# Optimization experiments

Measured on AMD Instinct MI355X. Metric: run time of the kernel, lower is better.

Reference implementation:

```python
import jax, jax.numpy as jnp
import numpy as np

B, C, D, Q = 256, 1000, 128, 262144
PROTO_M = 0.99   # args.proto_m
TEMP = 0.01      # hardcoded temperature in forward


def setup_inputs() -> dict:
    key = jax.random.key(0)
    ks = jax.random.split(key, 8)
    return {
        'q': jax.random.normal(ks[0], (B, D), jnp.float32),
        'k': jax.random.normal(ks[1], (B, D), jnp.float32),
        'output': jax.random.normal(ks[2], (B, C), jnp.float32),
        'output2': jax.random.normal(ks[3], (B, C), jnp.float32),
        'partial_Y': (jax.random.uniform(ks[4], (B, C)) < 0.1).astype(jnp.float32),
        'prototypes': jax.random.normal(ks[5], (C, D), jnp.float32),
        'queue': jax.random.normal(ks[6], (Q, D), jnp.float32),
        'queue_pseudo': jax.random.uniform(ks[7], (Q,), dtype=jnp.float32),
    }


def reference(q, k, output, output2, partial_Y, prototypes, queue, queue_pseudo):
    # pseudo-label selection: softmax over (detached logits * candidate mask) / T
    predicted_scores = jax.nn.softmax(jax.lax.stop_gradient(output) * partial_Y / TEMP, axis=1)
    pseudo_labels_b = jnp.argmax(predicted_scores, axis=1)  # [B] int

    # prototype scores use prototypes BEFORE the EMA update (mm snapshots values)
    logits_prot = jnp.matmul(jax.lax.stop_gradient(q), prototypes.T)  # [B, C]
    score_prot = jax.nn.softmax(logits_prot, axis=1)

    # sequential per-sample EMA scatter into prototypes (order-dependent on dup labels)
    q_detached = jax.lax.stop_gradient(q)

    def ema_step(protos, xs):
        feat, lab = xs
        new_row = protos[lab] * PROTO_M + (1.0 - PROTO_M) * feat
        return protos.at[lab].set(new_row), None

    protos, _ = jax.lax.scan(ema_step, prototypes, (q_detached, pseudo_labels_b))
    # F.normalize(p=2, dim=1) with eps=1e-12 clamp
    protos = protos / jnp.maximum(jnp.linalg.norm(protos, axis=1, keepdims=True), 1e-12)

    features = jnp.concatenate([q, k, queue], axis=0)  # [2B+Q, D]
    pseudo_labels = jnp.concatenate([
        pseudo_labels_b.astype(jnp.float32),
        pseudo_labels_b.astype(jnp.float32),
        queue_pseudo,
    ], axis=0)  # [2B+Q]

    return (output, output2, features, pseudo_labels, score_prot, protos)
```

## Files before the change

### kernel.cpp

```cpp
#include <hip/hip_runtime.h>
#include <math.h>

#define B 256
#define C 1000
#define D 128
#define QN 262144

#define OFF_FEAT   512000
#define OFF_LBL    34131968
#define OFF_SCORE  34394624
#define OFF_PROTO  34650624

#define N_Q4   (QN * D / 4)
#define N_O4   (B * C / 4)
#define N_F4   (B * D / 4)
#define N_P4   (QN / 4)

#define DST_Q4   ((OFF_FEAT + 2 * B * D) / 4)
#define DST_O24  (B * C / 4)
#define DST_QF4  (OFF_FEAT / 4)
#define DST_KF4  (OFF_FEAT / 4 + N_F4)
#define DST_P4   ((OFF_LBL + 2 * B) / 4)

#define SM_O2  (N_O4)
#define SM_Q   (2 * N_O4)
#define SM_K   (2 * N_O4 + N_F4)
#define SM_P   (2 * N_O4 + 2 * N_F4)
#define SM_TOT (2 * N_O4 + 2 * N_F4 + N_P4)

#define Q_TILES   (N_Q4 / 1024)
#define K1_TILES  640
#define POOL_BASE4 ((size_t)K1_TILES * 1024)
#define POOL_N4    ((size_t)(Q_TILES - K1_TILES) * 1024)

#define R_SP_END  256
#define R_EMA_END (R_SP_END + 250)
#define SM_BLKS   ((SM_TOT + 255) / 256)
#define R_SM_END  (R_EMA_END + SM_BLKS)
#define K2_GRID   2048
#define TOT_THR   ((size_t)K2_GRID * 256)

__global__ __launch_bounds__(256) void k1_kernel(
    const float* __restrict__ output,
    const float* __restrict__ partial_Y,
    const float4* __restrict__ queue,
    int* __restrict__ labels,
    float* __restrict__ out)
{
    const int tid = threadIdx.x;

    if (blockIdx.x >= B) {
        const size_t base = (size_t)(blockIdx.x - B) * 1024 + tid;
        float4* __restrict__ dst = (float4*)out + DST_Q4;
        float4 a = queue[base];
        float4 b = queue[base + 256];
        float4 c = queue[base + 512];
        float4 d = queue[base + 768];
        dst[base]       = a;
        dst[base + 256] = b;
        dst[base + 512] = c;
        dst[base + 768] = d;
        return;
    }

    const int b = blockIdx.x;
    const float* row = output + (size_t)b * C;
    const float* msk = partial_Y + (size_t)b * C;

    float best = -INFINITY;
    int bidx = C;
    for (int c = tid; c < C; c += 256) {
        float v = row[c] * msk[c];
        if (v > best) { best = v; bidx = c; }
    }

    __shared__ float sv[256];
    __shared__ int   si[256];
    sv[tid] = best; si[tid] = bidx;
    __syncthreads();
    for (int s = 128; s > 0; s >>= 1) {
        if (tid < s) {
            float v2 = sv[tid + s]; int i2 = si[tid + s];
            if (v2 > sv[tid] || (v2 == sv[tid] && i2 < si[tid])) {
                sv[tid] = v2; si[tid] = i2;
            }
        }
        __syncthreads();
    }
    if (tid == 0) {
        int lab = si[0];
        labels[b] = lab;
        float f = (float)lab;
        out[OFF_LBL + b]     = f;
        out[OFF_LBL + B + b] = f;
    }
}

__global__ __launch_bounds__(256) void k2_kernel(
    const float* __restrict__ q,
    const float* __restrict__ kk,
    const float* __restrict__ output,
    const float* __restrict__ output2,
    const float* __restrict__ prototypes,
    const float4* __restrict__ queue,
    const float* __restrict__ queue_pseudo,
    const int* __restrict__ labels,
    float* __restrict__ out)
{
    const int bid = blockIdx.x;
    const int tid = threadIdx.x;

    __shared__ float logits[C];
    __shared__ float red[256];
    __shared__ float qs[D];
    __shared__ int   lab[B];
    __shared__ float ss[256];

    if (bid < R_SP_END) {
        const int b = bid;
        if (tid < D) qs[tid] = q[(size_t)b * D + tid];
        __syncthreads();

        for (int c = tid; c < C; c += 256) {
            const float4* p4 = (const float4*)(prototypes + (size_t)c * D);
            const float4* q4 = (const float4*)qs;
            float acc = 0.f;
            #pragma unroll
            for (int d = 0; d < D / 4; ++d) {
                float4 pv = p4[d];
                float4 qv = q4[d];
                acc += pv.x * qv.x + pv.y * qv.y + pv.z * qv.z + pv.w * qv.w;
            }
            logits[c] = acc;
        }
        __syncthreads();

        float lm = -INFINITY;
        for (int c = tid; c < C; c += 256) lm = fmaxf(lm, logits[c]);
        red[tid] = lm;
        __syncthreads();
        for (int s = 128; s > 0; s >>= 1) {
            if (tid < s) red[tid] = fmaxf(red[tid], red[tid + s]);
            __syncthreads();
        }
        const float m = red[0];
        __syncthreads();

        float psum = 0.f;
        for (int c = tid; c < C; c += 256) {
            float e = expf(logits[c] - m);
            logits[c] = e;
            psum += e;
        }
        red[tid] = psum;
        __syncthreads();
        for (int s = 128; s > 0; s >>= 1) {
            if (tid < s) red[tid] += red[tid + s];
            __syncthreads();
        }
        const float denom = red[0];

        for (int c = tid; c < C; c += 256)
            out[OFF_SCORE + (size_t)b * C + c] = logits[c] / denom;
    }
    else if (bid < R_EMA_END) {
        const int ebid = bid - R_SP_END;
        const int half = tid >> 7;
        const int d    = tid & 127;
        for (int i = tid; i < B; i += 256) lab[i] = labels[i];
        __syncthreads();

        #pragma unroll
        for (int kcl = 0; kcl < 2; ++kcl) {
            const int c = 4 * ebid + 2 * kcl + half;
            float val = prototypes[(size_t)c * D + d];
            #pragma unroll 8
            for (int b = 0; b < B; ++b) {
                if (lab[b] == c) {
                    val = val * 0.99f + 0.01f * q[(size_t)b * D + d];
                }
            }
            ss[tid] = val * val;
            __syncthreads();
            for (int s = 64; s > 0; s >>= 1) {
                if (d < s) ss[tid] += ss[tid + s];
                __syncthreads();
            }
            float r = fmaxf(sqrtf(ss[half * 128]), 1e-12f);
            out[OFF_PROTO + (size_t)c * D + d] = val / r;
            __syncthreads();
        }
    }
    else if (bid < R_SM_END) {
        const size_t i = (size_t)(bid - R_EMA_END) * 256 + tid;
        float4* __restrict__ out4 = (float4*)out;
        if (i < SM_O2)       out4[i]                     = ((const float4*)output)[i];
        else if (i < SM_Q)   out4[DST_O24 + (i - SM_O2)] = ((const float4*)output2)[i - SM_O2];
        else if (i < SM_K)   out4[DST_QF4 + (i - SM_Q)]  = ((const float4*)q)[i - SM_Q];
        else if (i < SM_P)   out4[DST_KF4 + (i - SM_K)]  = ((const float4*)kk)[i - SM_K];
        else if (i < SM_TOT) out4[DST_P4 + (i - SM_P)]   = ((const float4*)queue_pseudo)[i - SM_P];
    }

    const float4* __restrict__ srcq = queue + POOL_BASE4;
    float4* __restrict__ dstq = (float4*)out + DST_Q4 + POOL_BASE4;
    const size_t gid = (size_t)bid * 256 + tid;
    size_t i = gid;
    for (; i + 3 * TOT_THR < POOL_N4; i += 4 * TOT_THR) {
        float4 a = srcq[i];
        float4 b = srcq[i +     TOT_THR];
        float4 c = srcq[i + 2 * TOT_THR];
        float4 d = srcq[i + 3 * TOT_THR];
        dstq[i]               = a;
        dstq[i +     TOT_THR] = b;
        dstq[i + 2 * TOT_THR] = c;
        dstq[i + 3 * TOT_THR] = d;
    }
    for (; i < POOL_N4; i += TOT_THR)
        dstq[i] = srcq[i];
}

extern "C" void kernel_launch(void* const* d_in, const int* in_sizes, int n_in,
                              void* d_out, int out_size, void* d_ws, size_t ws_size,
                              hipStream_t stream) {
    const float* q            = (const float*)d_in[0];
    const float* k            = (const float*)d_in[1];
    const float* output       = (const float*)d_in[2];
    const float* output2      = (const float*)d_in[3];
    const float* partial_Y    = (const float*)d_in[4];
    const float* prototypes   = (const float*)d_in[5];
    const float* queue        = (const float*)d_in[6];
    const float* queue_pseudo = (const float*)d_in[7];

    float* out  = (float*)d_out;
    int* labels = (int*)d_ws;

    k1_kernel<<<B + K1_TILES, 256, 0, stream>>>(
        output, partial_Y, (const float4*)queue, labels, out);

    k2_kernel<<<K2_GRID, 256, 0, stream>>>(
        q, k, output, output2, prototypes,
        (const float4*)queue, queue_pseudo, labels, out);
}
```

Before: 270.7 us.

## Split work into three kernels: independent work first, EMA, then queue copy

```diff
diff --git a/kernel.cpp b/kernel.cpp
--- a/kernel.cpp
+++ b/kernel.cpp
@@ -33,91 +33,68 @@
 #define POOL_BASE4 ((size_t)K1_TILES * 1024)
 #define POOL_N4    ((size_t)(Q_TILES - K1_TILES) * 1024)
 
-#define R_SP_END  256
-#define R_EMA_END (R_SP_END + 250)
+#define R1_SP     256
+#define R1_SM     512
 #define SM_BLKS   ((SM_TOT + 255) / 256)
-#define R_SM_END  (R_EMA_END + SM_BLKS)
-#define K2_GRID   2048
-#define TOT_THR   ((size_t)K2_GRID * 256)
+#define R1_CP     (R1_SM + SM_BLKS)
+#define K1_GRID   (R1_CP + K1_TILES)
+
+#define K3_GRID   4096
 
 __global__ __launch_bounds__(256) void k1_kernel(
-    const float* __restrict__ output,
-    const float* __restrict__ partial_Y,
-    const float4* __restrict__ queue,
-    int* __restrict__ labels,
-    float* __restrict__ out)
-{
-    const int tid = threadIdx.x;
-
-    if (blockIdx.x >= B) {
-        const size_t base = (size_t)(blockIdx.x - B) * 1024 + tid;
-        float4* __restrict__ dst = (float4*)out + DST_Q4;
-        float4 a = queue[base];
-        float4 b = queue[base + 256];
-        float4 c = queue[base + 512];
-        float4 d = queue[base + 768];
-        dst[base]       = a;
-        dst[base + 256] = b;
-        dst[base + 512] = c;
-        dst[base + 768] = d;
-        return;
-    }
-
-    const int b = blockIdx.x;
-    const float* row = output + (size_t)b * C;
-    const float* msk = partial_Y + (size_t)b * C;
-
-    float best = -INFINITY;
-    int bidx = C;
-    for (int c = tid; c < C; c += 256) {
-        float v = row[c] * msk[c];
-        if (v > best) { best = v; bidx = c; }
-    }
-
-    __shared__ float sv[256];
-    __shared__ int   si[256];
-    sv[tid] = best; si[tid] = bidx;
-    __syncthreads();
-    for (int s = 128; s > 0; s >>= 1) {
-        if (tid < s) {
-            float v2 = sv[tid + s]; int i2 = si[tid + s];
-            if (v2 > sv[tid] || (v2 == sv[tid] && i2 < si[tid])) {
-                sv[tid] = v2; si[tid] = i2;
-            }
-        }
-        __syncthreads();
-    }
-    if (tid == 0) {
-        int lab = si[0];
-        labels[b] = lab;
-        float f = (float)lab;
-        out[OFF_LBL + b]     = f;
-        out[OFF_LBL + B + b] = f;
-    }
-}
-
-__global__ __launch_bounds__(256) void k2_kernel(
     const float* __restrict__ q,
     const float* __restrict__ kk,
     const float* __restrict__ output,
     const float* __restrict__ output2,
+    const float* __restrict__ partial_Y,
     const float* __restrict__ prototypes,
     const float4* __restrict__ queue,
     const float* __restrict__ queue_pseudo,
-    const int* __restrict__ labels,
+    int* __restrict__ labels,
     float* __restrict__ out)
 {
     const int bid = blockIdx.x;
     const int tid = threadIdx.x;
-
-    __shared__ float logits[C];
-    __shared__ float red[256];
-    __shared__ float qs[D];
-    __shared__ int   lab[B];
-    __shared__ float ss[256];
-
-    if (bid < R_SP_END) {
-        const int b = bid;
+    __shared__ float smem[1384];
+
+    if (bid < B) {
+        float* sv = smem;
+        int*   si = (int*)(smem + 256);
+        const float* row = output + (size_t)bid * C;
+        const float* msk = partial_Y + (size_t)bid * C;
+
+        float best = -INFINITY;
+        int bidx = C;
+        for (int c = tid; c < C; c += 256) {
+            float v = row[c] * msk[c];
+            if (v > best) { best = v; bidx = c; }
+        }
+        sv[tid] = best; si[tid] = bidx;
+        __syncthreads();
+        for (int s = 128; s > 0; s >>= 1) {
+            if (tid < s) {
+                float v2 = sv[tid + s]; int i2 = si[tid + s];
+                if (v2 > sv[tid] || (v2 == sv[tid] && i2 < si[tid])) {
+                    sv[tid] = v2; si[tid] = i2;
+                }
+            }
+            __syncthreads();
+        }
+        if (tid == 0) {
+            int lab = si[0];
+            labels[bid] = lab;
+            float f = (float)lab;
+            out[OFF_LBL + bid]     = f;
+            out[OFF_LBL + B + bid] = f;
+        }
+        return;
+    }
+
+    if (bid < R1_SM) {
+        const int b = bid - R1_SP;
+        float* logits = smem;
+        float* red    = smem + C;
+        float* qs     = smem + C + 256;
         if (tid < D) qs[tid] = q[(size_t)b * D + tid];
         __syncthreads();
 
@@ -162,61 +139,77 @@
 
         for (int c = tid; c < C; c += 256)
             out[OFF_SCORE + (size_t)b * C + c] = logits[c] / denom;
-    }
-    else if (bid < R_EMA_END) {
-        const int ebid = bid - R_SP_END;
-        const int half = tid >> 7;
-        const int d    = tid & 127;
-        for (int i = tid; i < B; i += 256) lab[i] = labels[i];
-        __syncthreads();
-
-        #pragma unroll
-        for (int kcl = 0; kcl < 2; ++kcl) {
-            const int c = 4 * ebid + 2 * kcl + half;
-            float val = prototypes[(size_t)c * D + d];
-            #pragma unroll 8
-            for (int b = 0; b < B; ++b) {
-                if (lab[b] == c) {
-                    val = val * 0.99f + 0.01f * q[(size_t)b * D + d];
-                }
-            }
-            ss[tid] = val * val;
-            __syncthreads();
-            for (int s = 64; s > 0; s >>= 1) {
-                if (d < s) ss[tid] += ss[tid + s];
-                __syncthreads();
-            }
-            float r = fmaxf(sqrtf(ss[half * 128]), 1e-12f);
-            out[OFF_PROTO + (size_t)c * D + d] = val / r;
-            __syncthreads();
-        }
-    }
-    else if (bid < R_SM_END) {
-        const size_t i = (size_t)(bid - R_EMA_END) * 256 + tid;
+        return;
+    }
+
+    if (bid < R1_CP) {
+        const size_t i = (size_t)(bid - R1_SM) * 256 + tid;
         float4* __restrict__ out4 = (float4*)out;
         if (i < SM_O2)       out4[i]                     = ((const float4*)output)[i];
         else if (i < SM_Q)   out4[DST_O24 + (i - SM_O2)] = ((const float4*)output2)[i - SM_O2];
         else if (i < SM_K)   out4[DST_QF4 + (i - SM_Q)]  = ((const float4*)q)[i - SM_Q];
         else if (i < SM_P)   out4[DST_KF4 + (i - SM_K)]  = ((const float4*)kk)[i - SM_K];
         else if (i < SM_TOT) out4[DST_P4 + (i - SM_P)]   = ((const float4*)queue_pseudo)[i - SM_P];
-    }
-
-    const float4* __restrict__ srcq = queue + POOL_BASE4;
-    float4* __restrict__ dstq = (float4*)out + DST_Q4 + POOL_BASE4;
-    const size_t gid = (size_t)bid * 256 + tid;
-    size_t i = gid;
-    for (; i + 3 * TOT_THR < POOL_N4; i += 4 * TOT_THR) {
-        float4 a = srcq[i];
-        float4 b = srcq[i +     TOT_THR];
-        float4 c = srcq[i + 2 * TOT_THR];
-        float4 d = srcq[i + 3 * TOT_THR];
-        dstq[i]               = a;
-        dstq[i +     TOT_THR] = b;
-        dstq[i + 2 * TOT_THR] = c;
-        dstq[i + 3 * TOT_THR] = d;
-    }
-    for (; i < POOL_N4; i += TOT_THR)
-        dstq[i] = srcq[i];
+        return;
+    }
+
+    const size_t base = (size_t)(bid - R1_CP) * 1024 + tid;
+    float4* __restrict__ dst = (float4*)out + DST_Q4;
+    float4 a = queue[base];
+    float4 b = queue[base + 256];
+    float4 c = queue[base + 512];
+    float4 d = queue[base + 768];
+    dst[base]       = a;
+    dst[base + 256] = b;
+    dst[base + 512] = c;
+    dst[base + 768] = d;
+}
+
+__global__ __launch_bounds__(256) void ema_kernel(
+    const float* __restrict__ q,
+    const float* __restrict__ prototypes,
+    const int* __restrict__ labels,
+    float* __restrict__ out)
+{
+    const int ebid = blockIdx.x;
+    const int tid  = threadIdx.x;
+    const int half = tid >> 7;
+    const int d    = tid & 127;
+
+    __shared__ int   lab[B];
+    __shared__ float ss[256];
+    for (int i = tid; i < B; i += 256) lab[i] = labels[i];
+    __syncthreads();
+
+    #pragma unroll
+    for (int kcl = 0; kcl < 2; ++kcl) {
+        const int c = 4 * ebid + 2 * kcl + half;
+        float val = prototypes[(size_t)c * D + d];
+        #pragma unroll 8
+        for (int b = 0; b < B; ++b) {
+            if (lab[b] == c) {
+                val = val * 0.99f + 0.01f * q[(size_t)b * D + d];
+            }
+        }
+        ss[tid] = val * val;
+        __syncthreads();
+        for (int s = 64; s > 0; s >>= 1) {
+            if (d < s) ss[tid] += ss[tid + s];
+            __syncthreads();
+        }
+        float r = fmaxf(sqrtf(ss[half * 128]), 1e-12f);
+        out[OFF_PROTO + (size_t)c * D + d] = val / r;
+        __syncthreads();
+    }
+}
+
+__global__ __launch_bounds__(256) void copy_kernel(
+    const float4* __restrict__ src, float4* __restrict__ dst)
+{
+    const size_t stride = (size_t)gridDim.x * blockDim.x;
+    for (size_t i = (size_t)blockIdx.x * blockDim.x + threadIdx.x;
+         i < POOL_N4; i += stride)
+        dst[i] = src[i];
 }
 
 extern "C" void kernel_launch(void* const* d_in, const int* in_sizes, int n_in,
@@ -234,10 +227,13 @@
     float* out  = (float*)d_out;
     int* labels = (int*)d_ws;
 
-    k1_kernel<<<B + K1_TILES, 256, 0, stream>>>(
-        output, partial_Y, (const float4*)queue, labels, out);
-
-    k2_kernel<<<K2_GRID, 256, 0, stream>>>(
-        q, k, output, output2, prototypes,
+    k1_kernel<<<K1_GRID, 256, 0, stream>>>(
+        q, k, output, output2, partial_Y, prototypes,
         (const float4*)queue, queue_pseudo, labels, out);
-}
+
+    ema_kernel<<<C / 4, 256, 0, stream>>>(q, prototypes, labels, out);
+
+    copy_kernel<<<K3_GRID, 256, 0, stream>>>(
+        (const float4*)queue + POOL_BASE4,
+        (float4*)out + DST_Q4 + POOL_BASE4);
+}
```

Result: slower. 304.3 us (+12.4%).
